# Performance work log

Measured on AMD Instinct MI355X. Metric: run time of the kernel, lower is better.

Reference implementation:

```python
import jax, jax.numpy as jnp
import numpy as np

DIM = 512; HEADS = 8; DH = 64; CHUNK = 64; DHID = DH * 4; MAX_LR = 1.0; EPS = 1e-6


def rmsnorm(x, w):
    return x * jax.lax.rsqrt(jnp.mean(x * x, axis=-1, keepdims=True) + EPS) * w


def mem_forward(params, x):
    # MemoryMLP(depth=2, expansion=4) wrapped in ResidualNorm
    nw, w0, w1 = params
    h = rmsnorm(x, nw)
    y = jax.nn.gelu(h @ w0) @ w1
    return y + x


def chunk_loss(params, k, lr, v):
    pred = mem_forward(params, k)            # (CHUNK, DH)
    loss = jnp.mean((pred - v) ** 2, axis=-1)  # per-token mse, (CHUNK,)
    return (loss * lr).sum(), loss


def assoc_scan(gates, inputs, prev=None):
    # h_t = g_t * h_{t-1} + x_t along axis=1 (chunks)
    def combine(a, b):
        g1, x1 = a; g2, x2 = b
        return g1 * g2, x2 + g2 * x1
    G, X = jax.lax.associative_scan(combine, (gates, inputs), axis=1)
    if prev is None:
        return X
    return X + G * prev[:, None]


def setup_inputs() -> dict:
    key = jax.random.key(0)
    ks = jax.random.split(key, 8)
    B, N = 2, 4096
    s = 0.02
    return {
        'seq': jax.random.normal(ks[0], (B, N, DIM), jnp.float32),
        'store_norm_w': jnp.ones((DIM,), jnp.float32),
        'Wk': jax.random.normal(ks[1], (DIM, HEADS * DH), jnp.float32) * s,
        'Wv': jax.random.normal(ks[2], (DIM, HEADS * DH), jnp.float32) * s,
        'Wstep': jax.random.normal(ks[3], (DIM, HEADS), jnp.float32) * s,
        'bstep': jnp.zeros((HEADS,), jnp.float32),
        'Wmom': jax.random.normal(ks[4], (DIM, HEADS), jnp.float32) * s,
        'bmom': jnp.zeros((HEADS,), jnp.float32),
        'Wdec': jax.random.normal(ks[5], (DIM, HEADS), jnp.float32) * s,
        'bdec': jnp.zeros((HEADS,), jnp.float32),
        'mem_norm_w': jnp.ones((HEADS, DH), jnp.float32),
        'mem_w0': jax.random.normal(ks[6], (HEADS, DH, DHID), jnp.float32) * s,
        'mem_w1': jax.random.normal(ks[7], (HEADS, DHID, DH), jnp.float32) * s,
    }


def reference(seq, store_norm_w, Wk, Wv, Wstep, bstep, Wmom, bmom, Wdec, bdec, mem_norm_w, mem_w0, mem_w1):
    B, N, _ = seq.shape
    nc = N // CHUNK
    bh = B * HEADS
    x = rmsnorm(seq, store_norm_w)                        # store pre-norm, (B,N,D)
    # per-token adaptive lr: 'b n h -> (b h) n', sigmoid * max_lr
    lr = jax.nn.sigmoid(x @ Wstep + bstep) * MAX_LR       # (B,N,H)
    lr = lr.transpose(0, 2, 1).reshape(bh, nc, CHUNK)
    # chunk-pooled rep (AveragePool) -> momentum / decay gates per chunk
    pooled = x.reshape(B, nc, CHUNK, DIM).mean(axis=2)    # (B,nc,D)
    mom = jax.nn.sigmoid(pooled @ Wmom + bmom).transpose(0, 2, 1).reshape(bh, nc, 1)
    decay = jax.nn.sigmoid(pooled @ Wdec + bdec).transpose(0, 2, 1).reshape(bh, nc, 1)

    def split(t):  # (B,N,H*DH) -> (bh, nc, CHUNK, DH)
        return t.reshape(B, N, HEADS, DH).transpose(0, 2, 1, 3).reshape(bh, nc, CHUNK, DH)
    k = split(x @ Wk)
    v = split(x @ Wv)

    # initial fast weights per (b h) stream: repeat 'h ... -> (b h) ...'
    params0 = (jnp.tile(mem_norm_w, (B, 1)),
               jnp.tile(mem_w0, (B, 1, 1)),
               jnp.tile(mem_w1, (B, 1, 1)))

    # per-chunk per-stream grads via vmap(grad) (all chunks share the initial weights)
    grad_fn = jax.grad(chunk_loss, has_aux=True)
    per_chunk = jax.vmap(grad_fn, in_axes=(None, 0, 0, 0))
    per_bh = jax.vmap(per_chunk, in_axes=(0, 0, 0, 0))
    grads, _ = per_bh(params0, k, lr, v)                  # tuple of (bh, nc, *shape)

    finals = []
    for g, w0 in zip(grads, params0):
        surprise = -g
        extra = (1,) * (g.ndim - 2)
        m = mom.reshape(bh, nc, *extra)
        d = decay.reshape(bh, nc, *extra)
        update = assoc_scan(m, surprise)                  # momentum scan, zero init
        wts = assoc_scan(1.0 - d, update, prev=w0)        # decay recurrence from init weights
        finals.append(wts[:, -1].reshape(bh, -1))
    return jnp.concatenate(finals, axis=-1)              # (bh, DH + DH*DHID + DHID*DH)
```

## Files before the change

### kernel.cpp

```cpp
#include <hip/hip_runtime.h>
#include <math.h>

typedef __attribute__((ext_vector_type(8)))  __bf16 bf16x8;
typedef __attribute__((ext_vector_type(4)))  float  f32x4;
typedef __attribute__((ext_vector_type(4)))  unsigned short ushort4v;
typedef __attribute__((ext_vector_type(8)))  unsigned short ushort8v;

#define MFMA16(acc, a, b) acc = __builtin_amdgcn_mfma_f32_16x16x32_bf16((a),(b),(acc),0,0,0)

__device__ inline unsigned short f2b(float f) {
    union { float f; unsigned int u; } v; v.f = f;
    unsigned int r = v.u + 0x7FFFu + ((v.u >> 16) & 1u);
    return (unsigned short)(r >> 16);
}
__device__ inline float b2f(unsigned short h) {
    union { unsigned int u; float f; } v; v.u = ((unsigned int)h) << 16;
    return v.f;
}
__device__ inline float tanh_fast(float z) {
    float e = __expf(2.0f * z);
    return 1.0f - 2.0f / (e + 1.0f);
}
__device__ inline float gelu_g(float x) {
    const float c0 = 0.7978845608028654f, c1 = 0.044715f;
    float z = c0 * x * (1.0f + c1 * x * x);
    return 0.5f * x * (1.0f + tanh_fast(z));
}
__device__ inline void gelu_both(float x, float& g, float& gp) {
    const float c0 = 0.7978845608028654f, c1 = 0.044715f;
    float x2 = x * x;
    float z  = c0 * x * (1.0f + c1 * x2);
    float t  = tanh_fast(z);
    g  = 0.5f * x * (1.0f + t);
    float dz = c0 * (1.0f + 3.0f * c1 * x2);
    gp = 0.5f * (1.0f + t) + 0.5f * x * (1.0f - t * t) * dz;
}
__device__ inline float sigmoidf(float x) { return 1.0f / (1.0f + __expf(-x)); }

__global__ __launch_bounds__(256) void k_wprep(
    const float* __restrict__ Wk, const float* __restrict__ Wv,
    const float* __restrict__ w0_g, const float* __restrict__ w1_g,
    const float* __restrict__ nw_g,
    unsigned short* __restrict__ WkvT, unsigned short* __restrict__ w0fT,
    unsigned short* __restrict__ w1T, unsigned short* __restrict__ w0N,
    unsigned short* __restrict__ w1N)
{
    const int bid = blockIdx.x, tid = threadIdx.x;
    __shared__ float tile[64][65];
    if (bid < 128) {
        int kt = bid >> 4, nt = bid & 15;
        const float* src = (nt < 8) ? Wk : Wv;
        int ncol0 = (nt & 7) * 64;
        for (int ii = 0; ii < 16; ++ii) {
            int idx = tid + ii * 256; int r = idx >> 6, cc = idx & 63;
            tile[r][cc] = src[(size_t)(kt * 64 + r) * 512 + ncol0 + cc];
        }
        __syncthreads();
        for (int ii = 0; ii < 16; ++ii) {
            int idx = tid + ii * 256; int r = idx >> 6, cc = idx & 63;
            WkvT[(size_t)(nt * 64 + r) * 512 + kt * 64 + cc] = f2b(tile[cc][r]);
        }
    } else if (bid < 160) {
        int q = bid - 128; int hh = q >> 2, it = q & 3;
        const float* w0h = w0_g + hh * 16384;
        for (int ii = 0; ii < 16; ++ii) {
            int idx = tid + ii * 256; int r = idx >> 6, cc = idx & 63;
            tile[r][cc] = w0h[r * 256 + it * 64 + cc];
        }
        __syncthreads();
        for (int ii = 0; ii < 16; ++ii) {
            int idx = tid + ii * 256; int r = idx >> 6, cc = idx & 63;
            w0fT[hh * 16384 + (it * 64 + r) * 64 + cc] = f2b(nw_g[hh * 64 + cc] * tile[cc][r]);
        }
    } else if (bid < 192) {
        int q = bid - 160; int hh = q >> 2, it = q & 3;
        const float* w1h = w1_g + hh * 16384;
        for (int ii = 0; ii < 16; ++ii) {
            int idx = tid + ii * 256; int r = idx >> 6, cc = idx & 63;
            tile[r][cc] = w1h[(it * 64 + r) * 64 + cc];
        }
        __syncthreads();
        for (int ii = 0; ii < 16; ++ii) {
            int idx = tid + ii * 256; int r = idx >> 6, cc = idx & 63;
            w1T[hh * 16384 + r * 256 + it * 64 + cc] = f2b(tile[cc][r]);
        }
    } else {
        int q = bid - 192;
        int gid = q * 2048 + tid * 8;
        const float* s; unsigned short* d;
        if (gid < 131072) { s = w0_g + gid; d = w0N + gid; }
        else              { s = w1_g + (gid - 131072); d = w1N + (gid - 131072); }
        #pragma unroll
        for (int jj = 0; jj < 8; ++jj) d[jj] = f2b(s[jj]);
    }
}

__global__ __launch_bounds__(256) void k_rms_lr(
    const float* __restrict__ seq, const float* __restrict__ wnorm,
    const float* __restrict__ Wstep, const float* __restrict__ bstep,
    unsigned short* __restrict__ xb, float* __restrict__ lrb)
{
    const int wid = threadIdx.x >> 6, lane = threadIdx.x & 63;
    const int t = blockIdx.x * 4 + wid;
    const float* row = seq + (size_t)t * 512 + lane * 8;
    float v[8];
    *(f32x4*)&v[0] = *(const f32x4*)row;
    *(f32x4*)&v[4] = *(const f32x4*)(row + 4);
    float ss = 0.f;
    #pragma unroll
    for (int j = 0; j < 8; ++j) ss += v[j] * v[j];
    #pragma unroll
    for (int o = 1; o < 64; o <<= 1) ss += __shfl_xor(ss, o);
    float rr = rsqrtf(ss * (1.0f / 512.0f) + 1e-6f);
    const float* wn = wnorm + lane * 8;
    ushort8v xs;
    float acc[8] = {0.f,0.f,0.f,0.f,0.f,0.f,0.f,0.f};
    #pragma unroll
    for (int j = 0; j < 8; ++j) {
        float xf = v[j] * rr * wn[j];
        xs[j] = f2b(xf);
        const float* wrow = Wstep + (size_t)(lane * 8 + j) * 8;
        #pragma unroll
        for (int h = 0; h < 8; ++h) acc[h] = fmaf(xf, wrow[h], acc[h]);
    }
    *(ushort8v*)(xb + (size_t)t * 512 + lane * 8) = xs;
    #pragma unroll
    for (int h = 0; h < 8; ++h) {
        #pragma unroll
        for (int o = 1; o < 64; o <<= 1) acc[h] += __shfl_xor(acc[h], o);
    }
    if (lane == 0) {
        #pragma unroll
        for (int h = 0; h < 8; ++h) lrb[(size_t)t * 8 + h] = sigmoidf(acc[h] + bstep[h]);
    }
}

__global__ __launch_bounds__(256) void k_poolgates(
    const unsigned short* __restrict__ xb,
    const float* __restrict__ Wmom, const float* __restrict__ bmom,
    const float* __restrict__ Wdec, const float* __restrict__ bdec,
    float* __restrict__ momout, float* __restrict__ decout)
{
    __shared__ float sP[4][512];
    __shared__ float pooled[512];
    const int bc = blockIdx.x, tid = threadIdx.x;
    const int q = tid >> 6, lane = tid & 63, d0 = lane * 8;
    float p[8] = {0.f,0.f,0.f,0.f,0.f,0.f,0.f,0.f};
    for (int tt = 0; tt < 16; ++tt) {
        int t = q * 16 + tt;
        ushort8v v = *(const ushort8v*)(xb + (size_t)(bc * 64 + t) * 512 + d0);
        #pragma unroll
        for (int j = 0; j < 8; ++j) p[j] += b2f(v[j]);
    }
    #pragma unroll
    for (int j = 0; j < 8; ++j) sP[q][d0 + j] = p[j];
    __syncthreads();
    #pragma unroll
    for (int half = 0; half < 2; ++half) {
        int d = tid + half * 256;
        pooled[d] = (sP[0][d] + sP[1][d] + sP[2][d] + sP[3][d]) * (1.0f / 64.0f);
    }
    __syncthreads();
    if (tid < 64) {
        const int h = tid & 7, dd0 = tid >> 3;
        float pm = 0.f, pd = 0.f;
        #pragma unroll 8
        for (int it = 0; it < 64; ++it) {
            int d = dd0 + it * 8; float pv = pooled[d];
            pm = fmaf(pv, Wmom[d * 8 + h], pm);
            pd = fmaf(pv, Wdec[d * 8 + h], pd);
        }
        #pragma unroll
        for (int o = 8; o < 64; o <<= 1) { pm += __shfl_xor(pm, o); pd += __shfl_xor(pd, o); }
        if (tid < 8) {
            momout[(size_t)bc * 8 + h] = sigmoidf(pm + bmom[h]);
            decout[(size_t)bc * 8 + h] = sigmoidf(pd + bdec[h]);
        }
    }
}

__global__ __launch_bounds__(256) void k_proj(
    const unsigned short* __restrict__ xb, const unsigned short* __restrict__ WkvT,
    unsigned short* __restrict__ kbh, unsigned short* __restrict__ vb)
{
    __shared__ __attribute__((aligned(16))) unsigned short As[128][72];
    __shared__ __attribute__((aligned(16))) unsigned short Bs[128][72];
    const int tid = threadIdx.x;
    const int bm = blockIdx.x >> 3, bn = blockIdx.x & 7;
    const int m0 = bm * 128, n0 = bn * 128;
    const int wid = tid >> 6, lane = tid & 63, lg = lane >> 4, lo = lane & 15;
    const int wm = wid >> 1, wn = wid & 1;
    f32x4 acc[4][4];
    #pragma unroll
    for (int i = 0; i < 4; ++i)
        #pragma unroll
        for (int j = 0; j < 4; ++j) acc[i][j] = (f32x4)0.f;

    for (int k0 = 0; k0 < 512; k0 += 64) {
        #pragma unroll
        for (int ii = 0; ii < 4; ++ii) {
            int e0 = tid * 32 + ii * 8;
            int r = e0 >> 6, c = e0 & 63;
            *(bf16x8*)&As[r][c] = *(const bf16x8*)(xb   + (size_t)(m0 + r) * 512 + k0 + c);
            *(bf16x8*)&Bs[r][c] = *(const bf16x8*)(WkvT + (size_t)(n0 + r) * 512 + k0 + c);
        }
        __syncthreads();
        #pragma unroll
        for (int ks = 0; ks < 2; ++ks) {
            bf16x8 aF[4], bF[4];
            #pragma unroll
            for (int mt = 0; mt < 4; ++mt) aF[mt] = *(const bf16x8*)&As[wm * 64 + mt * 16 + lo][ks * 32 + 8 * lg];
            #pragma unroll
            for (int nt = 0; nt < 4; ++nt) bF[nt] = *(const bf16x8*)&Bs[wn * 64 + nt * 16 + lo][ks * 32 + 8 * lg];
            #pragma unroll
            for (int mt = 0; mt < 4; ++mt)
                #pragma unroll
                for (int nt = 0; nt < 4; ++nt) MFMA16(acc[mt][nt], aF[mt], bF[nt]);
        }
        __syncthreads();
    }
    #pragma unroll
    for (int mt = 0; mt < 4; ++mt)
        #pragma unroll
        for (int nt = 0; nt < 4; ++nt)
            #pragma unroll
            for (int r = 0; r < 4; ++r) {
                int row = m0 + wm * 64 + mt * 16 + lg * 4 + r;
                int col = n0 + wn * 64 + nt * 16 + lo;
                unsigned short val = f2b(acc[mt][nt][r]);
                if (col < 512) kbh[(size_t)row * 512 + col] = val;
                else           vb[(size_t)row * 512 + col - 512] = val;
            }
}

__global__ void k_coeff(const float* __restrict__ mom, const float* __restrict__ dec,
                        float* __restrict__ coeff, float* __restrict__ Aout)
{
    __shared__ float sm[1024], sd[1024];
    int tid = threadIdx.x;
    #pragma unroll
    for (int i = 0; i < 4; ++i) {
        int idx = (tid + i * 64) * 4;
        *(f32x4*)&sm[idx] = *(const f32x4*)&mom[idx];
        *(f32x4*)&sd[idx] = *(const f32x4*)&dec[idx];
    }
    __syncthreads();
    int s = tid;
    if (s >= 16) return;
    int b = s >> 3, h = s & 7;
    float P = 1.f, S = 1.f;
    coeff[s * 64 + 63] = 1.f;
    for (int cc = 62; cc >= 0; --cc) {
        float Dn = 1.f - sd[(b * 64 + cc + 1) * 8 + h];
        float Mn = sm[(b * 64 + cc + 1) * 8 + h];
        P *= Dn;
        S = P + Mn * S;
        coeff[s * 64 + cc] = S;
    }
    float D0 = 1.f - sd[(b * 64) * 8 + h];
    Aout[s] = P * D0;
}

__global__ __launch_bounds__(256) void k_fwd(
    const unsigned short* __restrict__ kbh, const unsigned short* __restrict__ vb,
    const float* __restrict__ lrb, const float* __restrict__ cfb,
    const unsigned short* __restrict__ w0fT, const unsigned short* __restrict__ w1T,
    unsigned short* __restrict__ uws, unsigned short* __restrict__ ews,
    unsigned short* __restrict__ ewsT)
{
    __shared__ __attribute__((aligned(16))) unsigned short sU[64][72];
    __shared__ __attribute__((aligned(16))) unsigned short sG[2][64][72];
    const int tid = threadIdx.x, blk = blockIdx.x;
    const int s = blk >> 6, c = blk & 63;
    const int b = s >> 3, h = s & 7;
    const int row0 = b * 4096 + c * 64;
    const int wid = tid >> 6, lane = tid & 63, lg = lane >> 4, lo = lane & 15;
    const size_t ubase = (size_t)blk * 4096;

    {
        int r = tid >> 2, c0 = (tid & 3) * 16;
        const unsigned short* kr = kbh + (size_t)(row0 + r) * 512 + h * 64 + c0;
        ushort8v k0 = *(const ushort8v*)kr;
        ushort8v k1 = *(const ushort8v*)(kr + 8);
        float kv[16];
        float ss = 0.f;
        #pragma unroll
        for (int j = 0; j < 8; ++j) { kv[j] = b2f(k0[j]); kv[8 + j] = b2f(k1[j]); }
        #pragma unroll
        for (int j = 0; j < 16; ++j) ss += kv[j] * kv[j];
        ss += __shfl_xor(ss, 1);
        ss += __shfl_xor(ss, 2);
        float rr = rsqrtf(ss * (1.0f / 64.0f) + 1e-6f);
        ushort8v u0, u1;
        #pragma unroll
        for (int j = 0; j < 8; ++j) { u0[j] = f2b(kv[j] * rr); u1[j] = f2b(kv[8 + j] * rr); }
        *(ushort8v*)&sU[r][c0]     = u0;
        *(ushort8v*)&sU[r][c0 + 8] = u1;
        *(ushort8v*)(uws + ubase + r * 64 + c0)     = u0;
        *(ushort8v*)(uws + ubase + r * 64 + c0 + 8) = u1;
    }
    __syncthreads();

    const unsigned short* w0h = w0fT + h * 16384;
    const unsigned short* w1h = w1T  + h * 16384;
    bf16x8 aF0 = *(const bf16x8*)&sU[wid * 16 + lo][8 * lg];
    bf16x8 aF1 = *(const bf16x8*)&sU[wid * 16 + lo][32 + 8 * lg];

    f32x4 yac[4];
    #pragma unroll
    for (int nt = 0; nt < 4; ++nt) yac[nt] = (f32x4)0.f;

    for (int is = 0; is < 4; ++is) {
        const int bi = is & 1;
        f32x4 a1[4];
        #pragma unroll
        for (int nt = 0; nt < 4; ++nt) a1[nt] = (f32x4)0.f;
        #pragma unroll
        for (int nt = 0; nt < 4; ++nt) {
            bf16x8 b0 = *(const bf16x8*)(w0h + (size_t)(is * 64 + nt * 16 + lo) * 64 + 8 * lg);
            bf16x8 b1 = *(const bf16x8*)(w0h + (size_t)(is * 64 + nt * 16 + lo) * 64 + 32 + 8 * lg);
            MFMA16(a1[nt], aF0, b0);
            MFMA16(a1[nt], aF1, b1);
        }
        #pragma unroll
        for (int nt = 0; nt < 4; ++nt)
            #pragma unroll
            for (int r = 0; r < 4; ++r) {
                int t = wid * 16 + lg * 4 + r;
                sG[bi][t][nt * 16 + lo] = f2b(gelu_g(a1[nt][r]));
            }
        __syncthreads();
        #pragma unroll
        for (int ks = 0; ks < 2; ++ks) {
            bf16x8 aW = *(const bf16x8*)(w1h + (size_t)(wid * 16 + lo) * 256 + is * 64 + ks * 32 + 8 * lg);
            #pragma unroll
            for (int nt = 0; nt < 4; ++nt) {
                bf16x8 bG = *(const bf16x8*)&sG[bi][nt * 16 + lo][ks * 32 + 8 * lg];
                MFMA16(yac[nt], aW, bG);
            }
        }
    }

    float coefv = cfb[s * 64 + c];
    ushort4v evs[4];
    #pragma unroll
    for (int nt = 0; nt < 4; ++nt) {
        int t = nt * 16 + lo; int grow = row0 + t;
        float sc = -coefv * lrb[(size_t)grow * 8 + h] * (2.0f / 64.0f);
        ushort4v k4 = *(const ushort4v*)(kbh + (size_t)grow * 512 + h * 64 + wid * 16 + lg * 4);
        ushort4v v4 = *(const ushort4v*)(vb  + (size_t)grow * 512 + h * 64 + wid * 16 + lg * 4);
        ushort4v ev;
        #pragma unroll
        for (int r = 0; r < 4; ++r)
            ev[r] = f2b(sc * (yac[nt][r] + b2f(k4[r]) - b2f(v4[r])));
        evs[nt] = ev;
        *(ushort4v*)(ews + ubase + t * 64 + wid * 16 + lg * 4) = ev;
    }

    #pragma unroll
    for (int nt = 0; nt < 4; ++nt)
        *(ushort4v*)&sG[0][nt * 16 + lo][wid * 16 + lg * 4] = evs[nt];
    __syncthreads();
    {
        int r2 = tid >> 2, c2 = (tid & 3) * 16;
        ushort8v o0, o1;
        #pragma unroll
        for (int jj = 0; jj < 8; ++jj) o0[jj] = sG[0][c2 + jj][r2];
        #pragma unroll
        for (int jj = 0; jj < 8; ++jj) o1[jj] = sG[0][c2 + 8 + jj][r2];
        *(ushort8v*)(ewsT + ubase + r2 * 64 + c2)     = o0;
        *(ushort8v*)(ewsT + ubase + r2 * 64 + c2 + 8) = o1;
    }
}

__global__ __launch_bounds__(256) void k_bwd(
    const unsigned short* __restrict__ uws, const unsigned short* __restrict__ ews,
    const unsigned short* __restrict__ ewsT,
    const unsigned short* __restrict__ w0fT, const unsigned short* __restrict__ w0N,
    const unsigned short* __restrict__ w1N, const float* __restrict__ nw_g,
    float* __restrict__ pws, float* __restrict__ gnwb)
{
    __shared__ __attribute__((aligned(16))) unsigned short sGT[2][64][72];
    __shared__ __attribute__((aligned(16))) unsigned short sDAT[2][64][72];
    __shared__ __attribute__((aligned(16))) unsigned short sDAN[2][64][68];
    const int tid = threadIdx.x, blk = blockIdx.x;
    const int s = blk >> 5, ksl = (blk >> 2) & 7, is = blk & 3;
    const int h = s & 7;
    const int wid = tid >> 6, lane = tid & 63, lg = lane >> 4, lo = lane & 15;

    f32x4 gw1a[4], gw0a[4];
    #pragma unroll
    for (int nt = 0; nt < 4; ++nt) { gw1a[nt] = (f32x4)0.f; gw0a[nt] = (f32x4)0.f; }
    float gnwp[4] = {0.f, 0.f, 0.f, 0.f};

    const unsigned short* w0fh = w0fT + h * 16384;
    const unsigned short* w0nh = w0N  + h * 16384;
    const unsigned short* w1nh = w1N  + h * 16384;

    for (int tt = 0; tt < 8; ++tt) {
        const int bi = tt & 1;
        const int chunk = ksl * 8 + tt;
        const size_t base = (size_t)(s * 64 + chunk) * 4096;

        unsigned short utg[16];
        #pragma unroll
        for (int ks = 0; ks < 2; ++ks)
            #pragma unroll
            for (int jj = 0; jj < 8; ++jj)
                utg[ks * 8 + jj] = uws[base + (size_t)(ks * 32 + 8 * lg + jj) * 64 + wid * 16 + lo];
        ushort4v u4n[4];
        #pragma unroll
        for (int nt = 0; nt < 4; ++nt)
            u4n[nt] = *(const ushort4v*)(uws + base + (size_t)(nt * 16 + lo) * 64 + wid * 16 + lg * 4);

        f32x4 a1[4];
        #pragma unroll
        for (int nt = 0; nt < 4; ++nt) a1[nt] = (f32x4)0.f;
        bf16x8 aF0 = *(const bf16x8*)(uws + base + (size_t)(wid * 16 + lo) * 64 + 8 * lg);
        bf16x8 aF1 = *(const bf16x8*)(uws + base + (size_t)(wid * 16 + lo) * 64 + 32 + 8 * lg);
        #pragma unroll
        for (int nt = 0; nt < 4; ++nt) {
            bf16x8 b0 = *(const bf16x8*)(w0fh + (size_t)(is * 64 + nt * 16 + lo) * 64 + 8 * lg);
            bf16x8 b1 = *(const bf16x8*)(w0fh + (size_t)(is * 64 + nt * 16 + lo) * 64 + 32 + 8 * lg);
            MFMA16(a1[nt], aF0, b0);
            MFMA16(a1[nt], aF1, b1);
        }
        float gpv[4][4];
        #pragma unroll
        for (int nt = 0; nt < 4; ++nt) {
            ushort4v gv;
            #pragma unroll
            for (int r = 0; r < 4; ++r) {
                float g, gp; gelu_both(a1[nt][r], g, gp);
                gv[r] = f2b(g); gpv[nt][r] = gp;
            }
            *(ushort4v*)&sGT[bi][nt * 16 + lo][wid * 16 + lg * 4] = gv;
        }

        f32x4 dga[4];
        #pragma unroll
        for (int nt = 0; nt < 4; ++nt) dga[nt] = (f32x4)0.f;
        bf16x8 eF0 = *(const bf16x8*)(ews + base + (size_t)(wid * 16 + lo) * 64 + 8 * lg);
        bf16x8 eF1 = *(const bf16x8*)(ews + base + (size_t)(wid * 16 + lo) * 64 + 32 + 8 * lg);
        #pragma unroll
        for (int nt = 0; nt < 4; ++nt) {
            bf16x8 b0 = *(const bf16x8*)(w1nh + (size_t)(is * 64 + nt * 16 + lo) * 64 + 8 * lg);
            bf16x8 b1 = *(const bf16x8*)(w1nh + (size_t)(is * 64 + nt * 16 + lo) * 64 + 32 + 8 * lg);
            MFMA16(dga[nt], eF0, b0);
            MFMA16(dga[nt], eF1, b1);
        }
        #pragma unroll
        for (int nt = 0; nt < 4; ++nt) {
            ushort4v dv;
            #pragma unroll
            for (int r = 0; r < 4; ++r) dv[r] = f2b(dga[nt][r] * gpv[nt][r]);
            *(ushort4v*)&sDAT[bi][nt * 16 + lo][wid * 16 + lg * 4] = dv;
            #pragma unroll
            for (int r = 0; r < 4; ++r) sDAN[bi][wid * 16 + lg * 4 + r][nt * 16 + lo] = dv[r];
        }
        __syncthreads();

        #pragma unroll
        for (int ks = 0; ks < 2; ++ks) {
            bf16x8 aG = *(const bf16x8*)&sGT[bi][wid * 16 + lo][ks * 32 + 8 * lg];
            #pragma unroll
            for (int nt = 0; nt < 4; ++nt) {
                bf16x8 bE = *(const bf16x8*)(ewsT + base + (size_t)(nt * 16 + lo) * 64 + ks * 32 + 8 * lg);
                MFMA16(gw1a[nt], aG, bE);
            }
        }
        #pragma unroll
        for (int ks = 0; ks < 2; ++ks) {
            union { ushort8v u; bf16x8 b; } cu;
            #pragma unroll
            for (int jj = 0; jj < 8; ++jj) cu.u[jj] = utg[ks * 8 + jj];
            #pragma unroll
            for (int nt = 0; nt < 4; ++nt) {
                bf16x8 bD = *(const bf16x8*)&sDAT[bi][nt * 16 + lo][ks * 32 + 8 * lg];
                MFMA16(gw0a[nt], cu.b, bD);
            }
        }
        f32x4 dht[4];
        #pragma unroll
        for (int nt = 0; nt < 4; ++nt) dht[nt] = (f32x4)0.f;
        #pragma unroll
        for (int ks = 0; ks < 2; ++ks) {
            bf16x8 aW0 = *(const bf16x8*)(w0nh + (size_t)(wid * 16 + lo) * 256 + is * 64 + ks * 32 + 8 * lg);
            #pragma unroll
            for (int nt = 0; nt < 4; ++nt) {
                bf16x8 bDA = *(const bf16x8*)&sDAN[bi][nt * 16 + lo][ks * 32 + 8 * lg];
                MFMA16(dht[nt], aW0, bDA);
            }
        }
        #pragma unroll
        for (int nt = 0; nt < 4; ++nt)
            #pragma unroll
            for (int r = 0; r < 4; ++r)
                gnwp[r] += b2f(u4n[nt][r]) * dht[nt][r];
    }

    size_t pb = (size_t)blk * 8192;
    #pragma unroll
    for (int nt = 0; nt < 4; ++nt)
        #pragma unroll
        for (int r = 0; r < 4; ++r)
            pws[pb + (size_t)(wid * 16 + lg * 4 + r) * 64 + nt * 16 + lo] = gw1a[nt][r];
    #pragma unroll
    for (int r = 0; r < 4; ++r) {
        float nwv = nw_g[h * 64 + wid * 16 + lg * 4 + r];
        #pragma unroll
        for (int nt = 0; nt < 4; ++nt)
            pws[pb + 4096 + (size_t)(wid * 16 + lg * 4 + r) * 64 + nt * 16 + lo] = nwv * gw0a[nt][r];
    }
    #pragma unroll
    for (int r = 0; r < 4; ++r) {
        #pragma unroll
        for (int o = 1; o < 16; o <<= 1) gnwp[r] += __shfl_xor(gnwp[r], o);
    }
    if (lo == 0) {
        #pragma unroll
        for (int r = 0; r < 4; ++r)
            gnwb[(size_t)blk * 64 + wid * 16 + lg * 4 + r] = gnwp[r];
    }
}

__global__ __launch_bounds__(256) void k_reduce(
    const float* __restrict__ pws, const float* __restrict__ gnwb,
    const float* __restrict__ Ab,
    const float* __restrict__ nw_g, const float* __restrict__ w0_g,
    const float* __restrict__ w1_g, float* __restrict__ out)
{
    int gid = blockIdx.x * 256 + threadIdx.x;
    if (gid >= 16 * 32832) return;
    int s = gid / 32832, r = gid % 32832;
    int h = s & 7;
    float A = Ab[s];
    float val;
    if (r < 64) {
        val = A * nw_g[h * 64 + r];
        #pragma unroll
        for (int ks = 0; ks < 8; ++ks)
            #pragma unroll
            for (int i2 = 0; i2 < 4; ++i2)
                val += gnwb[(size_t)(s * 32 + ks * 4 + i2) * 64 + r];
    } else if (r < 16448) {
        int rr = r - 64; int d = rr >> 8; int i = rr & 255; int i2 = i >> 6, iloc = i & 63;
        val = A * w0_g[h * 16384 + rr];
        #pragma unroll
        for (int ks = 0; ks < 8; ++ks)
            val += pws[(size_t)(s * 32 + ks * 4 + i2) * 8192 + 4096 + d * 64 + iloc];
    } else {
        int rr = r - 16448; int i = rr >> 6; int j = rr & 63; int i2 = i >> 6, iloc = i & 63;
        val = A * w1_g[h * 16384 + rr];
        #pragma unroll
        for (int ks = 0; ks < 8; ++ks)
            val += pws[(size_t)(s * 32 + ks * 4 + i2) * 8192 + iloc * 64 + j];
    }
    out[gid] = val;
}

extern "C" void kernel_launch(void* const* d_in, const int* in_sizes, int n_in,
                              void* d_out, int out_size, void* d_ws, size_t ws_size,
                              hipStream_t stream) {
    (void)in_sizes; (void)n_in; (void)out_size; (void)ws_size;
    const float* seq   = (const float*)d_in[0];
    const float* snw   = (const float*)d_in[1];
    const float* Wk    = (const float*)d_in[2];
    const float* Wv    = (const float*)d_in[3];
    const float* Wstep = (const float*)d_in[4];
    const float* bstep = (const float*)d_in[5];
    const float* Wmom  = (const float*)d_in[6];
    const float* bmom  = (const float*)d_in[7];
    const float* Wdec  = (const float*)d_in[8];
    const float* bdec  = (const float*)d_in[9];
    const float* nw_g  = (const float*)d_in[10];
    const float* w0_g  = (const float*)d_in[11];
    const float* w1_g  = (const float*)d_in[12];
    float* out = (float*)d_out;

    char* ws = (char*)d_ws;
    unsigned short* xb   = (unsigned short*)(ws + 0);
    unsigned short* uws  = (unsigned short*)(ws + 0);
    unsigned short* WkvT = (unsigned short*)(ws + 8388608);
    float*          gnwb = (float*)        (ws + 8388608);
    unsigned short* kbh  = (unsigned short*)(ws + 9437184);
    unsigned short* vb   = (unsigned short*)(ws + 17825792);
    float*          pws  = (float*)        (ws + 9437184);
    unsigned short* ews  = (unsigned short*)(ws + 26214400);
    unsigned short* ewsT = (unsigned short*)(ws + 34603008);
    unsigned short* w0fT = (unsigned short*)(ws + 42991616);
    unsigned short* w1T  = (unsigned short*)(ws + 43253760);
    unsigned short* w0N  = (unsigned short*)(ws + 43515904);
    unsigned short* w1N  = (unsigned short*)(ws + 43778048);
    float* lrb  = (float*)(ws + 44040192);
    float* momb = (float*)(ws + 44302336);
    float* decb = (float*)(ws + 44306432);
    float* cfb  = (float*)(ws + 44310528);
    float* Ab   = (float*)(ws + 44314624);

    k_wprep    <<<320, 256, 0, stream>>>(Wk, Wv, w0_g, w1_g, nw_g, WkvT, w0fT, w1T, w0N, w1N);
    k_rms_lr   <<<2048, 256, 0, stream>>>(seq, snw, Wstep, bstep, xb, lrb);
    k_poolgates<<<128, 256, 0, stream>>>(xb, Wmom, bmom, Wdec, bdec, momb, decb);
    k_proj     <<<512, 256, 0, stream>>>(xb, WkvT, kbh, vb);
    k_coeff    <<<1, 64, 0, stream>>>(momb, decb, cfb, Ab);
    k_fwd      <<<1024, 256, 0, stream>>>(kbh, vb, lrb, cfb, w0fT, w1T, uws, ews, ewsT);
    k_bwd      <<<512, 256, 0, stream>>>(uws, ews, ewsT, w0fT, w0N, w1N, nw_g, pws, gnwb);
    k_reduce   <<<2052, 256, 0, stream>>>(pws, gnwb, Ab, nw_g, w0_g, w1_g, out);
}
```

Measured before the change: 138.6 us.

## Split backward hidden slices finer, remap blocks across XCDs, raise MFMA priority

The backward kernel now splits the hidden dimension into 8 slices of 32 instead of 4 of 64, so it launches twice as many blocks with smaller accumulators and less shared memory, and it adds a 3-block occupancy hint. The reduce kernel is updated to the new partial-sum layout and sums 64 partials for the norm-weight gradient. Both forward and backward kernels remap block IDs so consecutive work items of one stream spread across the 8 XCDs, and s_setprio wraps the MFMA sections. The aim is more parallelism and occupancy in the backward pass, at the cost of reloading each chunk's u and e data twice as often and more reduction work.

```diff
diff --git a/kernel.cpp b/kernel.cpp
--- a/kernel.cpp
+++ b/kernel.cpp
@@ -270,12 +270,13 @@
 {
     __shared__ __attribute__((aligned(16))) unsigned short sU[64][72];
     __shared__ __attribute__((aligned(16))) unsigned short sG[2][64][72];
-    const int tid = threadIdx.x, blk = blockIdx.x;
-    const int s = blk >> 6, c = blk & 63;
+    const int tid = threadIdx.x, bid = blockIdx.x;
+    const int work = (bid & 7) * 128 + (bid >> 3);
+    const int s = work >> 6, c = work & 63;
     const int b = s >> 3, h = s & 7;
     const int row0 = b * 4096 + c * 64;
     const int wid = tid >> 6, lane = tid & 63, lg = lane >> 4, lo = lane & 15;
-    const size_t ubase = (size_t)blk * 4096;
+    const size_t ubase = (size_t)work * 4096;
 
     {
         int r = tid >> 2, c0 = (tid & 3) * 16;
@@ -315,6 +316,7 @@
         f32x4 a1[4];
         #pragma unroll
         for (int nt = 0; nt < 4; ++nt) a1[nt] = (f32x4)0.f;
+        __builtin_amdgcn_s_setprio(1);
         #pragma unroll
         for (int nt = 0; nt < 4; ++nt) {
             bf16x8 b0 = *(const bf16x8*)(w0h + (size_t)(is * 64 + nt * 16 + lo) * 64 + 8 * lg);
@@ -322,6 +324,7 @@
             MFMA16(a1[nt], aF0, b0);
             MFMA16(a1[nt], aF1, b1);
         }
+        __builtin_amdgcn_s_setprio(0);
         #pragma unroll
         for (int nt = 0; nt < 4; ++nt)
             #pragma unroll
@@ -330,6 +333,7 @@
                 sG[bi][t][nt * 16 + lo] = f2b(gelu_g(a1[nt][r]));
             }
         __syncthreads();
+        __builtin_amdgcn_s_setprio(1);
         #pragma unroll
         for (int ks = 0; ks < 2; ++ks) {
             bf16x8 aW = *(const bf16x8*)(w1h + (size_t)(wid * 16 + lo) * 256 + is * 64 + ks * 32 + 8 * lg);
@@ -339,6 +343,7 @@
                 MFMA16(yac[nt], aW, bG);
             }
         }
+        __builtin_amdgcn_s_setprio(0);
     }
 
     float coefv = cfb[s * 64 + c];
@@ -373,24 +378,25 @@
     }
 }
 
-__global__ __launch_bounds__(256) void k_bwd(
+__global__ __launch_bounds__(256, 3) void k_bwd(
     const unsigned short* __restrict__ uws, const unsigned short* __restrict__ ews,
     const unsigned short* __restrict__ ewsT,
     const unsigned short* __restrict__ w0fT, const unsigned short* __restrict__ w0N,
     const unsigned short* __restrict__ w1N, const float* __restrict__ nw_g,
     float* __restrict__ pws, float* __restrict__ gnwb)
 {
-    __shared__ __attribute__((aligned(16))) unsigned short sGT[2][64][72];
-    __shared__ __attribute__((aligned(16))) unsigned short sDAT[2][64][72];
-    __shared__ __attribute__((aligned(16))) unsigned short sDAN[2][64][68];
-    const int tid = threadIdx.x, blk = blockIdx.x;
-    const int s = blk >> 5, ksl = (blk >> 2) & 7, is = blk & 3;
+    __shared__ __attribute__((aligned(16))) unsigned short sGT[2][32][72];
+    __shared__ __attribute__((aligned(16))) unsigned short sDAT[2][32][72];
+    __shared__ __attribute__((aligned(16))) unsigned short sDAN[2][64][40];
+    const int tid = threadIdx.x, bid = blockIdx.x;
+    const int work = (bid & 7) * 128 + (bid >> 3);
+    const int s = work >> 6, ksl = (work >> 3) & 7, is = work & 7;
     const int h = s & 7;
     const int wid = tid >> 6, lane = tid & 63, lg = lane >> 4, lo = lane & 15;
 
-    f32x4 gw1a[4], gw0a[4];
-    #pragma unroll
-    for (int nt = 0; nt < 4; ++nt) { gw1a[nt] = (f32x4)0.f; gw0a[nt] = (f32x4)0.f; }
+    f32x4 gw1a[2], gw0a[2];
+    #pragma unroll
+    for (int nt = 0; nt < 2; ++nt) { gw1a[nt] = (f32x4)0.f; gw0a[nt] = (f32x4)0.f; }
     float gnwp[4] = {0.f, 0.f, 0.f, 0.f};
 
     const unsigned short* w0fh = w0fT + h * 16384;
@@ -413,21 +419,23 @@
         for (int nt = 0; nt < 4; ++nt)
             u4n[nt] = *(const ushort4v*)(uws + base + (size_t)(nt * 16 + lo) * 64 + wid * 16 + lg * 4);
 
-        f32x4 a1[4];
-        #pragma unroll
-        for (int nt = 0; nt < 4; ++nt) a1[nt] = (f32x4)0.f;
+        f32x4 a1[2];
+        #pragma unroll
+        for (int nt = 0; nt < 2; ++nt) a1[nt] = (f32x4)0.f;
         bf16x8 aF0 = *(const bf16x8*)(uws + base + (size_t)(wid * 16 + lo) * 64 + 8 * lg);
         bf16x8 aF1 = *(const bf16x8*)(uws + base + (size_t)(wid * 16 + lo) * 64 + 32 + 8 * lg);
-        #pragma unroll
-        for (int nt = 0; nt < 4; ++nt) {
-            bf16x8 b0 = *(const bf16x8*)(w0fh + (size_t)(is * 64 + nt * 16 + lo) * 64 + 8 * lg);
-            bf16x8 b1 = *(const bf16x8*)(w0fh + (size_t)(is * 64 + nt * 16 + lo) * 64 + 32 + 8 * lg);
+        __builtin_amdgcn_s_setprio(1);
+        #pragma unroll
+        for (int nt = 0; nt < 2; ++nt) {
+            bf16x8 b0 = *(const bf16x8*)(w0fh + (size_t)(is * 32 + nt * 16 + lo) * 64 + 8 * lg);
+            bf16x8 b1 = *(const bf16x8*)(w0fh + (size_t)(is * 32 + nt * 16 + lo) * 64 + 32 + 8 * lg);
             MFMA16(a1[nt], aF0, b0);
             MFMA16(a1[nt], aF1, b1);
         }
-        float gpv[4][4];
-        #pragma unroll
-        for (int nt = 0; nt < 4; ++nt) {
+        __builtin_amdgcn_s_setprio(0);
+        float gpv[2][4];
+        #pragma unroll
+        for (int nt = 0; nt < 2; ++nt) {
             ushort4v gv;
             #pragma unroll
             for (int r = 0; r < 4; ++r) {
@@ -437,20 +445,22 @@
             *(ushort4v*)&sGT[bi][nt * 16 + lo][wid * 16 + lg * 4] = gv;
         }
 
-        f32x4 dga[4];
-        #pragma unroll
-        for (int nt = 0; nt < 4; ++nt) dga[nt] = (f32x4)0.f;
+        f32x4 dga[2];
+        #pragma unroll
+        for (int nt = 0; nt < 2; ++nt) dga[nt] = (f32x4)0.f;
         bf16x8 eF0 = *(const bf16x8*)(ews + base + (size_t)(wid * 16 + lo) * 64 + 8 * lg);
         bf16x8 eF1 = *(const bf16x8*)(ews + base + (size_t)(wid * 16 + lo) * 64 + 32 + 8 * lg);
-        #pragma unroll
-        for (int nt = 0; nt < 4; ++nt) {
-            bf16x8 b0 = *(const bf16x8*)(w1nh + (size_t)(is * 64 + nt * 16 + lo) * 64 + 8 * lg);
-            bf16x8 b1 = *(const bf16x8*)(w1nh + (size_t)(is * 64 + nt * 16 + lo) * 64 + 32 + 8 * lg);
+        __builtin_amdgcn_s_setprio(1);
+        #pragma unroll
+        for (int nt = 0; nt < 2; ++nt) {
+            bf16x8 b0 = *(const bf16x8*)(w1nh + (size_t)(is * 32 + nt * 16 + lo) * 64 + 8 * lg);
+            bf16x8 b1 = *(const bf16x8*)(w1nh + (size_t)(is * 32 + nt * 16 + lo) * 64 + 32 + 8 * lg);
             MFMA16(dga[nt], eF0, b0);
             MFMA16(dga[nt], eF1, b1);
         }
-        #pragma unroll
-        for (int nt = 0; nt < 4; ++nt) {
+        __builtin_amdgcn_s_setprio(0);
+        #pragma unroll
+        for (int nt = 0; nt < 2; ++nt) {
             ushort4v dv;
             #pragma unroll
             for (int r = 0; r < 4; ++r) dv[r] = f2b(dga[nt][r] * gpv[nt][r]);
@@ -460,12 +470,13 @@
         }
         __syncthreads();
 
+        __builtin_amdgcn_s_setprio(1);
         #pragma unroll
         for (int ks = 0; ks < 2; ++ks) {
-            bf16x8 aG = *(const bf16x8*)&sGT[bi][wid * 16 + lo][ks * 32 + 8 * lg];
-            #pragma unroll
-            for (int nt = 0; nt < 4; ++nt) {
-                bf16x8 bE = *(const bf16x8*)(ewsT + base + (size_t)(nt * 16 + lo) * 64 + ks * 32 + 8 * lg);
+            bf16x8 aG = *(const bf16x8*)&sGT[bi][(wid & 1) * 16 + lo][ks * 32 + 8 * lg];
+            #pragma unroll
+            for (int nt = 0; nt < 2; ++nt) {
+                bf16x8 bE = *(const bf16x8*)(ewsT + base + (size_t)((wid >> 1) * 32 + nt * 16 + lo) * 64 + ks * 32 + 8 * lg);
                 MFMA16(gw1a[nt], aG, bE);
             }
         }
@@ -475,7 +486,7 @@
             #pragma unroll
             for (int jj = 0; jj < 8; ++jj) cu.u[jj] = utg[ks * 8 + jj];
             #pragma unroll
-            for (int nt = 0; nt < 4; ++nt) {
+            for (int nt = 0; nt < 2; ++nt) {
                 bf16x8 bD = *(const bf16x8*)&sDAT[bi][nt * 16 + lo][ks * 32 + 8 * lg];
                 MFMA16(gw0a[nt], cu.b, bD);
             }
@@ -483,15 +494,15 @@
         f32x4 dht[4];
         #pragma unroll
         for (int nt = 0; nt < 4; ++nt) dht[nt] = (f32x4)0.f;
-        #pragma unroll
-        for (int ks = 0; ks < 2; ++ks) {
-            bf16x8 aW0 = *(const bf16x8*)(w0nh + (size_t)(wid * 16 + lo) * 256 + is * 64 + ks * 32 + 8 * lg);
+        {
+            bf16x8 aW0 = *(const bf16x8*)(w0nh + (size_t)(wid * 16 + lo) * 256 + is * 32 + 8 * lg);
             #pragma unroll
             for (int nt = 0; nt < 4; ++nt) {
-                bf16x8 bDA = *(const bf16x8*)&sDAN[bi][nt * 16 + lo][ks * 32 + 8 * lg];
+                bf16x8 bDA = *(const bf16x8*)&sDAN[bi][nt * 16 + lo][8 * lg];
                 MFMA16(dht[nt], aW0, bDA);
             }
         }
+        __builtin_amdgcn_s_setprio(0);
         #pragma unroll
         for (int nt = 0; nt < 4; ++nt)
             #pragma unroll
@@ -499,28 +510,32 @@
                 gnwp[r] += b2f(u4n[nt][r]) * dht[nt][r];
     }
 
-    size_t pb = (size_t)blk * 8192;
-    #pragma unroll
-    for (int nt = 0; nt < 4; ++nt)
+    size_t pb = (size_t)work * 4096;
+    #pragma unroll
+    for (int nt = 0; nt < 2; ++nt)
+        #pragma unroll
+        for (int r = 0; r < 4; ++r) {
+            int ip = (wid & 1) * 16 + lg * 4 + r;
+            int j  = (wid >> 1) * 32 + nt * 16 + lo;
+            pws[pb + (size_t)ip * 64 + j] = gw1a[nt][r];
+        }
+    #pragma unroll
+    for (int r = 0; r < 4; ++r) {
+        int d = wid * 16 + lg * 4 + r;
+        float nwv = nw_g[h * 64 + d];
+        #pragma unroll
+        for (int nt = 0; nt < 2; ++nt)
+            pws[pb + 2048 + (size_t)d * 32 + nt * 16 + lo] = nwv * gw0a[nt][r];
+    }
+    #pragma unroll
+    for (int r = 0; r < 4; ++r) {
+        #pragma unroll
+        for (int o = 1; o < 16; o <<= 1) gnwp[r] += __shfl_xor(gnwp[r], o);
+    }
+    if (lo == 0) {
         #pragma unroll
         for (int r = 0; r < 4; ++r)
-            pws[pb + (size_t)(wid * 16 + lg * 4 + r) * 64 + nt * 16 + lo] = gw1a[nt][r];
-    #pragma unroll
-    for (int r = 0; r < 4; ++r) {
-        float nwv = nw_g[h * 64 + wid * 16 + lg * 4 + r];
-        #pragma unroll
-        for (int nt = 0; nt < 4; ++nt)
-            pws[pb + 4096 + (size_t)(wid * 16 + lg * 4 + r) * 64 + nt * 16 + lo] = nwv * gw0a[nt][r];
-    }
-    #pragma unroll
-    for (int r = 0; r < 4; ++r) {
-        #pragma unroll
-        for (int o = 1; o < 16; o <<= 1) gnwp[r] += __shfl_xor(gnwp[r], o);
-    }
-    if (lo == 0) {
-        #pragma unroll
-        for (int r = 0; r < 4; ++r)
-            gnwb[(size_t)blk * 64 + wid * 16 + lg * 4 + r] = gnwp[r];
+            gnwb[(size_t)work * 64 + wid * 16 + lg * 4 + r] = gnwp[r];
     }
 }
 
@@ -538,23 +553,20 @@
     float val;
     if (r < 64) {
         val = A * nw_g[h * 64 + r];
+        for (int q = 0; q < 64; ++q)
+            val += gnwb[(size_t)(s * 64 + q) * 64 + r];
+    } else if (r < 16448) {
+        int rr = r - 64; int d = rr >> 8; int i = rr & 255; int i2 = i >> 5, iloc = i & 31;
+        val = A * w0_g[h * 16384 + rr];
         #pragma unroll
         for (int ks = 0; ks < 8; ++ks)
-            #pragma unroll
-            for (int i2 = 0; i2 < 4; ++i2)
-                val += gnwb[(size_t)(s * 32 + ks * 4 + i2) * 64 + r];
-    } else if (r < 16448) {
-        int rr = r - 64; int d = rr >> 8; int i = rr & 255; int i2 = i >> 6, iloc = i & 63;
-        val = A * w0_g[h * 16384 + rr];
+            val += pws[(size_t)(s * 64 + ks * 8 + i2) * 4096 + 2048 + d * 32 + iloc];
+    } else {
+        int rr = r - 16448; int i = rr >> 6; int j = rr & 63; int i2 = i >> 5, iloc = i & 31;
+        val = A * w1_g[h * 16384 + rr];
         #pragma unroll
         for (int ks = 0; ks < 8; ++ks)
-            val += pws[(size_t)(s * 32 + ks * 4 + i2) * 8192 + 4096 + d * 64 + iloc];
-    } else {
-        int rr = r - 16448; int i = rr >> 6; int j = rr & 63; int i2 = i >> 6, iloc = i & 63;
-        val = A * w1_g[h * 16384 + rr];
-        #pragma unroll
-        for (int ks = 0; ks < 8; ++ks)
-            val += pws[(size_t)(s * 32 + ks * 4 + i2) * 8192 + iloc * 64 + j];
+            val += pws[(size_t)(s * 64 + ks * 8 + i2) * 4096 + iloc * 64 + j];
     }
     out[gid] = val;
 }
@@ -604,6 +616,6 @@
     k_proj     <<<512, 256, 0, stream>>>(xb, WkvT, kbh, vb);
     k_coeff    <<<1, 64, 0, stream>>>(momb, decb, cfb, Ab);
     k_fwd      <<<1024, 256, 0, stream>>>(kbh, vb, lrb, cfb, w0fT, w1T, uws, ews, ewsT);
-    k_bwd      <<<512, 256, 0, stream>>>(uws, ews, ewsT, w0fT, w0N, w1N, nw_g, pws, gnwb);
+    k_bwd      <<<1024, 256, 0, stream>>>(uws, ews, ewsT, w0fT, w0N, w1N, nw_g, pws, gnwb);
     k_reduce   <<<2052, 256, 0, stream>>>(pws, gnwb, Ab, nw_g, w0_g, w1_g, out);
 }
```

New measurement: 161.9 us. 16.8% more time.

## Pre-transpose u tiles for vectorized MFMA loads and store partials as bf16

Applied to the files above, without the earlier changes.

Adds a k_transu kernel that transposes each 64x64 bf16 u chunk into a separate buffer. k_bwd can then load the MFMA A operand for the gW0 product with two 16-byte vector loads instead of sixteen strided scalar gathers. Partial weight-gradient sums are now written as bf16 instead of fp32, halving k_bwd store traffic and k_reduce read traffic. The costs are an extra kernel launch with a full read and write of u, plus lower precision in the partial sums before reduction.

```diff
diff --git a/kernel.cpp b/kernel.cpp
--- a/kernel.cpp
+++ b/kernel.cpp
@@ -373,12 +373,28 @@
     }
 }
 
+__global__ __launch_bounds__(256) void k_transu(
+    const unsigned short* __restrict__ uws, unsigned short* __restrict__ uwsT)
+{
+    __shared__ unsigned short sT[64][72];
+    const int tid = threadIdx.x;
+    const size_t base = (size_t)blockIdx.x * 4096;
+    const int r = tid >> 2, c0 = (tid & 3) * 16;
+    ushort8v a0 = *(const ushort8v*)(uws + base + r * 64 + c0);
+    ushort8v a1 = *(const ushort8v*)(uws + base + r * 64 + c0 + 8);
+    #pragma unroll
+    for (int jj = 0; jj < 8; ++jj) { sT[c0 + jj][r] = a0[jj]; sT[c0 + 8 + jj][r] = a1[jj]; }
+    __syncthreads();
+    *(ushort8v*)(uwsT + base + r * 64 + c0)     = *(const ushort8v*)&sT[r][c0];
+    *(ushort8v*)(uwsT + base + r * 64 + c0 + 8) = *(const ushort8v*)&sT[r][c0 + 8];
+}
+
 __global__ __launch_bounds__(256) void k_bwd(
-    const unsigned short* __restrict__ uws, const unsigned short* __restrict__ ews,
-    const unsigned short* __restrict__ ewsT,
+    const unsigned short* __restrict__ uws, const unsigned short* __restrict__ uwsT,
+    const unsigned short* __restrict__ ews, const unsigned short* __restrict__ ewsT,
     const unsigned short* __restrict__ w0fT, const unsigned short* __restrict__ w0N,
     const unsigned short* __restrict__ w1N, const float* __restrict__ nw_g,
-    float* __restrict__ pws, float* __restrict__ gnwb)
+    unsigned short* __restrict__ pws, float* __restrict__ gnwb)
 {
     __shared__ __attribute__((aligned(16))) unsigned short sGT[2][64][72];
     __shared__ __attribute__((aligned(16))) unsigned short sDAT[2][64][72];
@@ -402,12 +418,8 @@
         const int chunk = ksl * 8 + tt;
         const size_t base = (size_t)(s * 64 + chunk) * 4096;
 
-        unsigned short utg[16];
-        #pragma unroll
-        for (int ks = 0; ks < 2; ++ks)
-            #pragma unroll
-            for (int jj = 0; jj < 8; ++jj)
-                utg[ks * 8 + jj] = uws[base + (size_t)(ks * 32 + 8 * lg + jj) * 64 + wid * 16 + lo];
+        bf16x8 aU0 = *(const bf16x8*)(uwsT + base + (size_t)(wid * 16 + lo) * 64 + 8 * lg);
+        bf16x8 aU1 = *(const bf16x8*)(uwsT + base + (size_t)(wid * 16 + lo) * 64 + 32 + 8 * lg);
         ushort4v u4n[4];
         #pragma unroll
         for (int nt = 0; nt < 4; ++nt)
@@ -471,13 +483,11 @@
         }
         #pragma unroll
         for (int ks = 0; ks < 2; ++ks) {
-            union { ushort8v u; bf16x8 b; } cu;
-            #pragma unroll
-            for (int jj = 0; jj < 8; ++jj) cu.u[jj] = utg[ks * 8 + jj];
+            bf16x8 aU = (ks == 0) ? aU0 : aU1;
             #pragma unroll
             for (int nt = 0; nt < 4; ++nt) {
                 bf16x8 bD = *(const bf16x8*)&sDAT[bi][nt * 16 + lo][ks * 32 + 8 * lg];
-                MFMA16(gw0a[nt], cu.b, bD);
+                MFMA16(gw0a[nt], aU, bD);
             }
         }
         f32x4 dht[4];
@@ -504,13 +514,13 @@
     for (int nt = 0; nt < 4; ++nt)
         #pragma unroll
         for (int r = 0; r < 4; ++r)
-            pws[pb + (size_t)(wid * 16 + lg * 4 + r) * 64 + nt * 16 + lo] = gw1a[nt][r];
+            pws[pb + (size_t)(wid * 16 + lg * 4 + r) * 64 + nt * 16 + lo] = f2b(gw1a[nt][r]);
     #pragma unroll
     for (int r = 0; r < 4; ++r) {
         float nwv = nw_g[h * 64 + wid * 16 + lg * 4 + r];
         #pragma unroll
         for (int nt = 0; nt < 4; ++nt)
-            pws[pb + 4096 + (size_t)(wid * 16 + lg * 4 + r) * 64 + nt * 16 + lo] = nwv * gw0a[nt][r];
+            pws[pb + 4096 + (size_t)(wid * 16 + lg * 4 + r) * 64 + nt * 16 + lo] = f2b(nwv * gw0a[nt][r]);
     }
     #pragma unroll
     for (int r = 0; r < 4; ++r) {
@@ -525,7 +535,7 @@
 }
 
 __global__ __launch_bounds__(256) void k_reduce(
-    const float* __restrict__ pws, const float* __restrict__ gnwb,
+    const unsigned short* __restrict__ pws, const float* __restrict__ gnwb,
     const float* __restrict__ Ab,
     const float* __restrict__ nw_g, const float* __restrict__ w0_g,
     const float* __restrict__ w1_g, float* __restrict__ out)
@@ -548,13 +558,13 @@
         val = A * w0_g[h * 16384 + rr];
         #pragma unroll
         for (int ks = 0; ks < 8; ++ks)
-            val += pws[(size_t)(s * 32 + ks * 4 + i2) * 8192 + 4096 + d * 64 + iloc];
+            val += b2f(pws[(size_t)(s * 32 + ks * 4 + i2) * 8192 + 4096 + d * 64 + iloc]);
     } else {
         int rr = r - 16448; int i = rr >> 6; int j = rr & 63; int i2 = i >> 6, iloc = i & 63;
         val = A * w1_g[h * 16384 + rr];
         #pragma unroll
         for (int ks = 0; ks < 8; ++ks)
-            val += pws[(size_t)(s * 32 + ks * 4 + i2) * 8192 + iloc * 64 + j];
+            val += b2f(pws[(size_t)(s * 32 + ks * 4 + i2) * 8192 + iloc * 64 + j]);
     }
     out[gid] = val;
 }
@@ -584,8 +594,9 @@
     unsigned short* WkvT = (unsigned short*)(ws + 8388608);
     float*          gnwb = (float*)        (ws + 8388608);
     unsigned short* kbh  = (unsigned short*)(ws + 9437184);
+    unsigned short* uwsT = (unsigned short*)(ws + 9437184);
     unsigned short* vb   = (unsigned short*)(ws + 17825792);
-    float*          pws  = (float*)        (ws + 9437184);
+    unsigned short* pws  = (unsigned short*)(ws + 17825792);
     unsigned short* ews  = (unsigned short*)(ws + 26214400);
     unsigned short* ewsT = (unsigned short*)(ws + 34603008);
     unsigned short* w0fT = (unsigned short*)(ws + 42991616);
@@ -604,6 +615,7 @@
     k_proj     <<<512, 256, 0, stream>>>(xb, WkvT, kbh, vb);
     k_coeff    <<<1, 64, 0, stream>>>(momb, decb, cfb, Ab);
     k_fwd      <<<1024, 256, 0, stream>>>(kbh, vb, lrb, cfb, w0fT, w1T, uws, ews, ewsT);
-    k_bwd      <<<512, 256, 0, stream>>>(uws, ews, ewsT, w0fT, w0N, w1N, nw_g, pws, gnwb);
+    k_transu   <<<1024, 256, 0, stream>>>(uws, uwsT);
+    k_bwd      <<<512, 256, 0, stream>>>(uws, uwsT, ews, ewsT, w0fT, w0N, w1N, nw_g, pws, gnwb);
     k_reduce   <<<2052, 256, 0, stream>>>(pws, gnwb, Ab, nw_g, w0_g, w1_g, out);
 }
```

Result: slower. 156.0 us (+12.5%).
